# Kernel tuning notes

Measured on AMD Instinct MI355X. Metric: run time of the kernel, lower is better.

The kernel has to match this reference:

```python
import jax, jax.numpy as jnp
import numpy as np

B, L, D, NH, NITEMS = 256, 200, 128, 2, 100000
HD = D // NH
LAMB = 0.6
NEG = -1e9

_PARAM_SHAPES = dict(
    item_emb=(NITEMS, D), pos_emb=(L, D),
    W_ei=(D, D), b_ei=(D,), W_eo=(D, D), b_eo=(D,), b_iah=(D,), b_oah=(D,),
    w_ih=(3 * D, 2 * D), b_ih=(3 * D,), w_hh=(3 * D, D), b_hh=(3 * D,),
    ln1_g=(D,), ln1_b=(D,),
    Wq=(D, D), bq=(D,), Wk=(D, D), bk=(D,), Wv=(D, D), bv=(D,), Wo=(D, D), bo=(D,),
    ln2_g=(D,), ln2_b=(D,), W1=(D, D), b1=(D,), W2=(D, D), b2=(D,),
    lnf_g=(D,), lnf_b=(D,),
)


def setup_inputs() -> dict:
    key = jax.random.key(0)
    ks = jax.random.split(key, len(_PARAM_SHAPES) + 2)
    stdv = 1.0 / np.sqrt(D)  # GCSAN._init_weights: uniform(-stdv, stdv) on ALL params
    p = {}
    for i, (name, shp) in enumerate(_PARAM_SHAPES.items()):
        p[name] = jax.random.uniform(ks[i], shp, jnp.float32, -stdv, stdv)
    lens = jax.random.randint(ks[-2], (B,), L // 4, L + 1)
    vals = jax.random.randint(ks[-1], (B, L), 1, NITEMS)
    # trailing zero padding, as the original break-on-zero loop assumes
    seqs = jnp.where(jnp.arange(L)[None, :] < lens[:, None], vals, 0).astype(jnp.int32)
    p['seqs'] = seqs
    p['lens'] = lens.astype(jnp.int32)
    return p


def _ln(x, g, b):
    mu = x.mean(-1, keepdims=True)
    var = ((x - mu) ** 2).mean(-1, keepdims=True)
    return (x - mu) / jnp.sqrt(var + 1e-5) * g + b


def _build_graph(seqs):
    # Vectorized replacement of _get_slice (per-row np.unique + adjacency build)
    def per_row(seq):
        s = jnp.sort(seq)
        first = jnp.concatenate([jnp.ones((1,), bool), s[1:] != s[:-1]])
        pos = jnp.cumsum(first) - 1  # compaction target of each first-occurrence
        items = jnp.zeros((L,), seq.dtype).at[jnp.where(first, pos, L)].set(s, mode='drop')
        n_u = first.sum()
        search = jnp.where(jnp.arange(L) < n_u, items, jnp.iinfo(jnp.int32).max)
        alias = jnp.searchsorted(search, seq).astype(jnp.int32)
        return items, alias
    items, alias = jax.vmap(per_row)(seqs)
    valid = seqs[:, 1:] > 0  # edge (i -> i+1) exists until first pad
    u = jnp.where(valid, alias[:, :-1], L)  # route masked edges to dummy row L
    v = jnp.where(valid, alias[:, 1:], L)
    bidx = jnp.arange(B)[:, None]
    uA = jnp.zeros((B, L + 1, L + 1), jnp.float32).at[bidx, u, v].set(1.0)[:, :L, :L]
    in_deg = jnp.maximum(uA.sum(1), 1.0)
    out_deg = jnp.maximum(uA.sum(2), 1.0)
    A_in = jnp.swapaxes(uA, 1, 2) / in_deg[:, :, None]   # A[i,j] = uA[j,i]/in_deg[i]
    A_out = uA / out_deg[:, :, None]                     # A[i,k] = uA[i,k]/out_deg[i]
    return alias, jnp.concatenate([A_in, A_out], axis=2), items  # A: [B, L, 2L]


def reference(item_emb, pos_emb, W_ei, b_ei, W_eo, b_eo, b_iah, b_oah,
              w_ih, b_ih, w_hh, b_hh, ln1_g, ln1_b, Wq, bq, Wk, bk, Wv, bv,
              Wo, bo, ln2_g, ln2_b, W1, b1, W2, b2, lnf_g, lnf_b, seqs, lens):
    alias, A, items = _build_graph(seqs)
    hidden = item_emb[items]  # [B, L, D]
    # SR-GNN gated cell, step = n_layers = 1
    for _ in range(1):
        h_in = jnp.einsum('bij,bjd->bid', A[:, :, :L], hidden @ W_ei.T + b_ei) + b_iah
        h_out = jnp.einsum('bij,bjd->bid', A[:, :, L:], hidden @ W_eo.T + b_eo) + b_oah
        gi = jnp.concatenate([h_in, h_out], -1) @ w_ih.T + b_ih
        gh = hidden @ w_hh.T + b_hh
        i_r, i_i, i_n = jnp.split(gi, 3, -1)
        h_r, h_i, h_n = jnp.split(gh, 3, -1)
        r = jax.nn.sigmoid(i_r + h_r)
        z = jax.nn.sigmoid(i_i + h_i)
        ng = jnp.tanh(i_n + r * h_n)
        hidden = ng + z * (hidden - ng)
    bidx = jnp.arange(B)
    seq_hidden = hidden[bidx[:, None], alias]  # alias-gather back to sequence order
    last_idx = lens - 1
    ht = seq_hidden[bidx, last_idx]
    x = seq_hidden + pos_emb[None, :, :]
    tl_mask = (seqs > 0)[:, :, None].astype(x.dtype)
    x = x * tl_mask
    causal = jnp.triu(jnp.ones((L, L), bool), 1)  # True = masked future (bidirectional=False)
    # SASRec-style block: ln -> MHA residual -> ln -> pointwise FFN residual
    q_in = _ln(x, ln1_g, ln1_b)
    heads = lambda t: t.reshape(B, L, NH, HD).transpose(0, 2, 1, 3)
    q = heads(q_in @ Wq.T + bq)
    k = heads(x @ Wk.T + bk)
    v = heads(x @ Wv.T + bv)
    sc = jnp.einsum('bhqd,bhkd->bhqk', q, k) / jnp.sqrt(jnp.asarray(HD, x.dtype))
    sc = jnp.where(causal[None, None], NEG, sc)
    attn = jax.nn.softmax(sc, -1)
    mo = jnp.einsum('bhqk,bhkd->bhqd', attn, v).transpose(0, 2, 1, 3).reshape(B, L, D) @ Wo.T + bo
    x = q_in + mo
    h = _ln(x, ln2_g, ln2_b)
    x = h + jax.nn.relu(h @ W1.T + b1) @ W2.T + b2
    x = x * tl_mask
    log_feats = _ln(x, lnf_g, lnf_b)
    out = log_feats[bidx, last_idx]
    return LAMB * out + (1.0 - LAMB) * ht
```

## Files before the change

### kernel.cpp

```cpp
#include <hip/hip_runtime.h>
#include <hip/hip_bf16.h>

#define Bb 256
#define Ll 200
#define Dd 128
#define BL (Bb*Ll)

typedef __hip_bfloat16 bf16;
typedef __attribute__((ext_vector_type(8))) short short8;
typedef __attribute__((ext_vector_type(4))) unsigned short ushort4v;
typedef __attribute__((ext_vector_type(4))) float floatx4;

__device__ __forceinline__ float b2f(bf16 v) { return __bfloat162float(v); }
__device__ __forceinline__ bf16  f2b(float v) { return __float2bfloat16(v); }
__device__ __forceinline__ float us2f(unsigned short u) { return __uint_as_float(((unsigned)u) << 16); }
__device__ __forceinline__ unsigned short f2us(float v) { bf16 t = f2b(v); return *(unsigned short*)&t; }
__device__ __forceinline__ float ldf(const void* p, int i, int f32) {
  return f32 ? ((const float*)p)[i] : b2f(((const bf16*)p)[i]);
}
__device__ __forceinline__ int detect_f32(const unsigned short* __restrict__ w) {
  unsigned short u = w[threadIdx.x & 63];
  return (__ballot(((u >> 7) & 0xFF) >= 0x7F) != 0ull) ? 1 : 0;
}
__device__ __forceinline__ void load_lds16(const void* g, void* l) {
  __builtin_amdgcn_global_load_lds((const __attribute__((address_space(1))) unsigned int*)g,
                                   (__attribute__((address_space(3))) unsigned int*)l, 16, 0, 0);
}

struct PackP {
  const void *W_ei,*W_eo,*w_ih,*w_hh,*Wk,*Wv,*Wqp,*Wop,*W1p,*W2p,*pos;
  const void *b_ei,*b_eo,*b_ih,*b_hh,*bk,*bv,*bqp,*bop,*b1p,*b2p,*biah,*boah;
  const void *ln1g,*ln1b,*ln2g,*ln2b,*lnfg,*lnfb;
  bf16 *cWhe,*cWih,*cWhh,*cWkv,*cWq,*cWo,*cW1,*cW2,*cPos;
  float *bias_he,*bias_gi,*bias_gh,*bias_kv,*cbq,*cbo,*cb1,*cb2,*cbiah,*cboah,*cln;
  const int* seqs;
  int *alias_g, *items_g; float *rin_g, *rout_g; unsigned *adj_g, *adjT_g;
};
__global__ __launch_bounds__(256) void k01(PackP p) {
  __shared__ alignas(16) int s[Ll];
  __shared__ int al[Ll], its[Ll];
  __shared__ alignas(4) unsigned char isf[Ll];
  __shared__ unsigned adjL[Ll*8], adjTL[Ll*8];
  if (blockIdx.x >= Bb) {
    int idx = (blockIdx.x - Bb) * 256 + threadIdx.x;
    int f32 = detect_f32((const unsigned short*)p.W_ei);
    if (idx < 131072) {
      if (idx < 32768) {
        int r = idx >> 7, c = idx & 127;
        p.cWhe[idx] = f2b(r < 128 ? ldf(p.W_ei, r*128+c, f32) : ldf(p.W_eo, (r-128)*128+c, f32));
      } else p.cWih[idx-32768] = f2b(ldf(p.w_ih, idx-32768, f32));
    } else if (idx < 278528) {
      if (idx < 180224)      p.cWhh[idx-131072] = f2b(ldf(p.w_hh, idx-131072, f32));
      else if (idx < 212992) {
        int i = idx - 180224; int r = i >> 7, c = i & 127;
        p.cWkv[i] = f2b(r < 128 ? ldf(p.Wk, r*128+c, f32) : ldf(p.Wv, (r-128)*128+c, f32));
      }
      else if (idx < 229376) p.cWq[idx-212992] = f2b(ldf(p.Wqp, idx-212992, f32));
      else if (idx < 245760) p.cWo[idx-229376] = f2b(ldf(p.Wop, idx-229376, f32));
      else if (idx < 262144) p.cW1[idx-245760] = f2b(ldf(p.W1p, idx-245760, f32));
      else                   p.cW2[idx-262144] = f2b(ldf(p.W2p, idx-262144, f32));
    } else if (idx < 304128) {
      p.cPos[idx-278528] = f2b(ldf(p.pos, idx-278528, f32));
    } else {
      int j = idx - 304128;
      if      (j < 256)  p.bias_he[j]     = (j<128) ? ldf(p.b_ei,j,f32) : ldf(p.b_eo,j-128,f32);
      else if (j < 640)  p.bias_gi[j-256] = ldf(p.b_ih, j-256, f32);
      else if (j < 1024) p.bias_gh[j-640] = ldf(p.b_hh, j-640, f32);
      else if (j < 1280) { int c=j-1024; p.bias_kv[c] = (c<128)? ldf(p.bk,c,f32): ldf(p.bv,c-128,f32); }
      else if (j < 1408) p.cbq[j-1280]   = ldf(p.bqp, j-1280, f32);
      else if (j < 1536) p.cbo[j-1408]   = ldf(p.bop, j-1408, f32);
      else if (j < 1664) p.cb1[j-1536]   = ldf(p.b1p, j-1536, f32);
      else if (j < 1792) p.cb2[j-1664]   = ldf(p.b2p, j-1664, f32);
      else if (j < 1920) p.cbiah[j-1792] = ldf(p.biah, j-1792, f32);
      else if (j < 2048) p.cboah[j-1920] = ldf(p.boah, j-1920, f32);
      else {
        int i = j - 2048, g = i >> 7, c2 = i & 127;
        const void* s6 = g==0?p.ln1g: g==1?p.ln1b: g==2?p.ln2g: g==3?p.ln2b: g==4?p.lnfg: p.lnfb;
        p.cln[i] = ldf(s6, c2, f32);
      }
    }
    return;
  }
  int b = blockIdx.x, t = threadIdx.x;
  if (t < Ll) s[t] = p.seqs[b*Ll + t];
  for (int i = t; i < Ll*8; i += 256) { adjL[i] = 0u; adjTL[i] = 0u; }
  __syncthreads();
  const int4* s4 = (const int4*)s;
  if (t < Ll) {
    int v = s[t]; int dup = 0;
    int nb = t >> 2;
    for (int j4 = 0; j4 < nb; j4++) {
      int4 sv = s4[j4];
      dup |= (sv.x==v) | (sv.y==v) | (sv.z==v) | (sv.w==v);
    }
    for (int j = nb*4; j < t; j++) dup |= (s[j]==v);
    isf[t] = dup ? 0 : 1; its[t] = 0;
  }
  __syncthreads();
  const unsigned* isfw = (const unsigned*)isf;
  if (t < Ll) {
    int v = s[t], r = 0;
    for (int j4 = 0; j4 < Ll/4; j4++) {
      int4 sv = s4[j4];
      unsigned fw = isfw[j4];
      r += ((fw & 0xffu)       && sv.x < v);
      r += ((fw & 0xff00u)     && sv.y < v);
      r += ((fw & 0xff0000u)   && sv.z < v);
      r += ((fw & 0xff000000u) && sv.w < v);
    }
    al[t] = r;
  }
  __syncthreads();
  if (t < Ll && isf[t]) its[al[t]] = s[t];
  if (t < Ll-1 && s[t+1] > 0) {
    int u = al[t], v = al[t+1];
    atomicOr(&adjL [u*8 + (v >> 5)], 1u << (v & 31));
    atomicOr(&adjTL[v*8 + (u >> 5)], 1u << (u & 31));
  }
  __syncthreads();
  if (t < Ll) {
    int od = 0, id = 0;
    for (int wd = 0; wd < 7; wd++) { od += __popc(adjL[t*8+wd]); id += __popc(adjTL[t*8+wd]); }
    p.rout_g [b*Ll + t] = 1.0f / (float)max(od, 1);
    p.rin_g  [b*Ll + t] = 1.0f / (float)max(id, 1);
    p.alias_g[b*Ll + t] = al[t];
    p.items_g[b*Ll + t] = its[t];
  }
  for (int i = t; i < Ll*8; i += 256) { p.adj_g[b*Ll*8 + i] = adjL[i]; p.adjT_g[b*Ll*8 + i] = adjTL[i]; }
}

__global__ __launch_bounds__(256) void k2_gather(const void* __restrict__ emb, const void* __restrict__ wei,
    const int* __restrict__ items_g, bf16* __restrict__ hidden)
{
  int idx = blockIdx.x * 256 + threadIdx.x;
  int f32 = detect_f32((const unsigned short*)wei);
  int n = idx >> 4, jv = idx & 15;
  int it = items_g[n];
  short8 o;
  if (f32) {
    const float* e = (const float*)emb + (size_t)it * 128 + jv * 8;
#pragma unroll
    for (int j = 0; j < 8; j++) o[j] = (short)f2us(e[j]);
  } else {
    o = ((const short8*)((const bf16*)emb + (size_t)it * 128))[jv];
  }
  ((short8*)hidden)[idx] = o;
}

template<int K>
__global__ __launch_bounds__(256) void gemm6(const bf16* __restrict__ A, const bf16* __restrict__ W,
    const float* __restrict__ bias,
    bf16* __restrict__ out_lo, int Nlo, bf16* __restrict__ out_hi, int Nhi, int split)
{
  __shared__ short As[128*128];
  __shared__ short Ws[128*128];
  int t = threadIdx.x;
  int wave = t >> 6, lane = t & 63;
  int q = lane >> 4, mr = lane & 15;
  int wm = wave & 1, wn = wave >> 1;
  int m0 = blockIdx.x * 128, n0 = blockIdx.y * 128;
  int srow = lane >> 4;
  int c16 = lane & 15;
  floatx4 acc[4][4] = {};
  for (int k0 = 0; k0 < K; k0 += 128) {
#pragma unroll
    for (int i = 0; i < 8; i++) {
      int seg = wave*8 + i;
      int r = seg*4 + srow;
      int gch = c16 ^ (r & 15);
      load_lds16(A + (size_t)(m0 + r) * K + k0 + gch*8, &As[seg*512]);
      load_lds16(W + (size_t)(n0 + r) * K + k0 + gch*8, &Ws[seg*512]);
    }
    __syncthreads();
#pragma unroll
    for (int kk = 0; kk < 4; kk++) {
      short8 af[4], wf[4];
#pragma unroll
      for (int i = 0; i < 4; i++) {
        int row = wm*64 + i*16 + mr;
        af[i] = *(const short8*)(&As[row*128 + ((kk*4+q) ^ (row&15))*8]);
      }
#pragma unroll
      for (int j = 0; j < 4; j++) {
        int row = wn*64 + j*16 + mr;
        wf[j] = *(const short8*)(&Ws[row*128 + ((kk*4+q) ^ (row&15))*8]);
      }
#pragma unroll
      for (int i = 0; i < 4; i++)
#pragma unroll
        for (int j = 0; j < 4; j++)
          acc[i][j] = __builtin_amdgcn_mfma_f32_16x16x32_bf16(wf[j], af[i], acc[i][j], 0, 0, 0);
    }
    if (k0 + 128 < K) __syncthreads();
  }
#pragma unroll
  for (int j = 0; j < 4; j++) {
    int ng = n0 + wn*64 + j*16 + q*4;
    floatx4 bs = *(const floatx4*)(bias + ng);
    bf16* outp; int col, stride;
    if (ng < split) { outp = out_lo; col = ng; stride = Nlo; }
    else            { outp = out_hi; col = ng - split; stride = Nhi; }
#pragma unroll
    for (int i = 0; i < 4; i++) {
      int m = m0 + wm*64 + i*16 + mr;
      ushort4v o;
#pragma unroll
      for (int e = 0; e < 4; e++) o[e] = f2us(acc[i][j][e] + bs[e]);
      *(ushort4v*)(outp + (size_t)m * stride + col) = o;
    }
  }
}

__global__ __launch_bounds__(256) void k3_agg(const bf16* __restrict__ he,
    const unsigned* __restrict__ adj_g, const unsigned* __restrict__ adjT_g,
    const float* __restrict__ rin_g, const float* __restrict__ rout_g,
    const float* __restrict__ cbiah, const float* __restrict__ cboah, bf16* __restrict__ hio)
{
  int b = blockIdx.x / 25, chunk = blockIdx.x % 25;
  int wave = threadIdx.x >> 6, lane = threadIdx.x & 63;
  bool isIn = lane < 32;
  int c = isIn ? 4*lane : 128 + 4*(lane-32);
  const bf16* heb = he + (size_t)b * Ll * 256;
  bf16* hiob = hio + (size_t)b * Ll * 256;
  float bias0 = isIn ? cbiah[c]   : cboah[c-128];
  float bias1 = isIn ? cbiah[c+1] : cboah[c-127];
  float bias2 = isIn ? cbiah[c+2] : cboah[c-126];
  float bias3 = isIn ? cbiah[c+3] : cboah[c-125];
#pragma unroll
  for (int s = 0; s < 2; s++) {
    int i = chunk*8 + wave + 4*s;
    const unsigned* mrow = (isIn ? adjT_g : adj_g) + ((size_t)b*Ll + i) * 8;
    float a0=0.f, a1=0.f, a2=0.f, a3=0.f;
    for (int wd = 0; wd < 7; wd++) {
      unsigned bits = mrow[wd];
      while (bits) {
        int j = (wd << 5) + __builtin_ctz(bits); bits &= bits - 1;
        ushort4v h4 = *(const ushort4v*)(heb + (size_t)j*256 + c);
        a0 += us2f(h4.x); a1 += us2f(h4.y); a2 += us2f(h4.z); a3 += us2f(h4.w);
      }
    }
    float r = isIn ? rin_g[b*Ll + i] : rout_g[b*Ll + i];
    ushort4v o;
    o.x = f2us(bias0 + r*a0); o.y = f2us(bias1 + r*a1);
    o.z = f2us(bias2 + r*a2); o.w = f2us(bias3 + r*a3);
    *(ushort4v*)(hiob + (size_t)i*256 + c) = o;
  }
}

__global__ __launch_bounds__(256) void k45(const bf16* __restrict__ gi, const bf16* __restrict__ gh,
    const bf16* __restrict__ hidden, const int* __restrict__ alias_g,
    const int* __restrict__ seqs, const int* __restrict__ lens,
    const bf16* __restrict__ cPos, bf16* __restrict__ x, float* __restrict__ ht)
{
  __shared__ bf16 hnew[Ll*64];
  __shared__ int aliasL[Ll];
  __shared__ unsigned char validL[Ll];
  int b = blockIdx.x >> 1, half = blockIdx.x & 1;
  int t = threadIdx.x;
  if (t < Ll) { aliasL[t] = alias_g[b*Ll + t]; validL[t] = seqs[b*Ll + t] > 0; }
  int li = lens[b] - 1;
  for (int u = t; u < Ll*8; u += 256) {
    int n = u >> 3, grp = u & 7;
    int j8 = half*8 + grp;
    const short8* gin = (const short8*)(gi + ((size_t)b*Ll + n) * 384);
    const short8* ghn = (const short8*)(gh + ((size_t)b*Ll + n) * 384);
    short8 vir = gin[j8], vii = gin[16+j8], vnn = gin[32+j8];
    short8 whr = ghn[j8], whi = ghn[16+j8], whn = ghn[32+j8];
    short8 hv  = ((const short8*)(hidden + ((size_t)b*Ll + n) * Dd))[j8];
    short8 o;
#pragma unroll
    for (int e = 0; e < 8; e++) {
      float ir = us2f((unsigned short)vir[e]), ii = us2f((unsigned short)vii[e]), inn = us2f((unsigned short)vnn[e]);
      float hr = us2f((unsigned short)whr[e]), hi = us2f((unsigned short)whi[e]), hn = us2f((unsigned short)whn[e]);
      float r  = 1.f / (1.f + __expf(-(ir + hr)));
      float z  = 1.f / (1.f + __expf(-(ii + hi)));
      float arg = inn + r * hn;
      float ex = __expf(-2.f * arg);
      float ng = (1.f - ex) / (1.f + ex);
      float h  = us2f((unsigned short)hv[e]);
      o[e] = (short)f2us(ng + z * (h - ng));
    }
    *(short8*)&hnew[n*64 + grp*8] = o;
  }
  __syncthreads();
  for (int u = t; u < Ll*8; u += 256) {
    int tpos = u >> 3, grp = u & 7;
    int a = aliasL[tpos];
    short8 sh8 = *(const short8*)&hnew[a*64 + grp*8];
    short8 pv = ((const short8*)(cPos + tpos * Dd))[half*8 + grp];
    bool valid = validL[tpos];
    bool isLast = (tpos == li);
    short8 o;
#pragma unroll
    for (int e = 0; e < 8; e++) {
      float sh = us2f((unsigned short)sh8[e]);
      o[e] = valid ? (short)f2us(sh + us2f((unsigned short)pv[e])) : (short)0;
      if (isLast) ht[b*Dd + half*64 + grp*8 + e] = sh;
    }
    ((short8*)(x + ((size_t)b*Ll + tpos) * Dd))[half*8 + grp] = o;
  }
}

struct FinalP {
  const bf16 *x, *kv; const float* ht;
  const bf16 *cWq, *cWo, *cW1, *cW2;
  const float *cbq, *cbo, *cb1, *cb2, *cln;
  const int* lens; const void* wei;
  void* out;
};
__device__ __forceinline__ float dot128i(const bf16* __restrict__ wrow, const float* __restrict__ vin) {
  const short8* wr = (const short8*)wrow;
  float a0=0.f, a1=0.f, a2=0.f, a3=0.f;
#pragma unroll
  for (int kk = 0; kk < 4; kk++) {
    short8 w0 = wr[kk*4+0], w1 = wr[kk*4+1], w2 = wr[kk*4+2], w3 = wr[kk*4+3];
#pragma unroll
    for (int j = 0; j < 8; j++) {
      a0 += vin[kk*32 +      j] * us2f((unsigned short)w0[j]);
      a1 += vin[kk*32 + 8  + j] * us2f((unsigned short)w1[j]);
      a2 += vin[kk*32 + 16 + j] * us2f((unsigned short)w2[j]);
      a3 += vin[kk*32 + 24 + j] * us2f((unsigned short)w3[j]);
    }
  }
  return (a0+a1)+(a2+a3);
}
__device__ __forceinline__ float wave_sum(float v) {
#pragma unroll
  for (int m = 1; m < 64; m <<= 1) v += __shfl_xor(v, m, 64);
  return v;
}
__device__ __forceinline__ float wave_max(float v) {
#pragma unroll
  for (int m = 1; m < 64; m <<= 1) v = fmaxf(v, __shfl_xor(v, m, 64));
  return v;
}
__global__ __launch_bounds__(256) void k7_final(FinalP p)
{
  __shared__ float sred[8];
  __shared__ float qin[128], qv[128], aout[128], hh[128], f1[128];
  __shared__ float pb0[256], pb1[256];
  __shared__ floatx4 av4[8][32];
  int b = blockIdx.x, t = threadIdx.x, c = t;
  int w = t >> 6, ln = t & 63;
  int li = p.lens[b] - 1;
  int f32 = detect_f32((const unsigned short*)p.wei);
  float xv = (c < 128) ? b2f(p.x[((size_t)b*Ll + li) * Dd + c]) : 0.f;
  float s = wave_sum(xv), s2 = wave_sum(xv*xv);
  if (ln == 0) { sred[w] = s; sred[4+w] = s2; }
  __syncthreads();
  float mu = (sred[0]+sred[1]+sred[2]+sred[3]) * (1.f/128.f);
  float ms = (sred[4]+sred[5]+sred[6]+sred[7]) * (1.f/128.f);
  float rs = rsqrtf(fmaxf(ms - mu*mu, 0.f) + 1e-5f);
  __syncthreads();
  if (c < 128) qin[c] = (xv - mu) * rs * p.cln[c] + p.cln[128+c];
  __syncthreads();
  if (c < 128) qv[c] = p.cbq[c] + dot128i(p.cWq + c*128, qin);
  __syncthreads();
  const bf16* kvb = p.kv + (size_t)b * Ll * 256;
  float s0 = -3.0e38f, s1 = -3.0e38f;
  if (t <= li) {
    const short8* kr = (const short8*)(kvb + (size_t)t*256);
    float a00=0.f,a01=0.f,a10=0.f,a11=0.f;
#pragma unroll
    for (int kk = 0; kk < 4; kk++) {
      short8 k0 = kr[kk*2], k1 = kr[kk*2+1], k2 = kr[8+kk*2], k3 = kr[8+kk*2+1];
#pragma unroll
      for (int j = 0; j < 8; j++) {
        a00 += qv[kk*16 + j]      * us2f((unsigned short)k0[j]);
        a01 += qv[kk*16 + 8 + j]  * us2f((unsigned short)k1[j]);
        a10 += qv[64 + kk*16 + j]     * us2f((unsigned short)k2[j]);
        a11 += qv[64 + kk*16 + 8 + j] * us2f((unsigned short)k3[j]);
      }
    }
    s0 = (a00+a01) * 0.125f; s1 = (a10+a11) * 0.125f;
  }
  float m0 = wave_max(s0), m1 = wave_max(s1);
  if (ln == 0) { sred[w] = m0; sred[4+w] = m1; }
  __syncthreads();
  m0 = fmaxf(fmaxf(sred[0],sred[1]), fmaxf(sred[2],sred[3]));
  m1 = fmaxf(fmaxf(sred[4],sred[5]), fmaxf(sred[6],sred[7]));
  __syncthreads();
  float e0 = (t <= li) ? __expf(s0 - m0) : 0.f;
  float e1 = (t <= li) ? __expf(s1 - m1) : 0.f;
  pb0[t] = e0; pb1[t] = e1;
  float l0 = wave_sum(e0), l1 = wave_sum(e1);
  if (ln == 0) { sred[w] = l0; sred[4+w] = l1; }
  __syncthreads();
  l0 = sred[0]+sred[1]+sred[2]+sred[3];
  l1 = sred[4]+sred[5]+sred[6]+sred[7];
  {
    int part = t >> 5, cq = t & 31, ch = cq * 4;
    int cnt = li + 1, cpp = (cnt + 7) >> 3;
    int j0 = part * cpp, j1 = min(j0 + cpp, cnt);
    const float* pbh = (ch < 64) ? pb0 : pb1;
    float a0=0.f,a1=0.f,a2=0.f,a3=0.f;
#pragma unroll 4
    for (int j = j0; j < j1; j++) {
      ushort4v v4 = *(const ushort4v*)(kvb + (size_t)j*256 + 128 + ch);
      float pw = pbh[j];
      a0 += pw*us2f(v4.x); a1 += pw*us2f(v4.y); a2 += pw*us2f(v4.z); a3 += pw*us2f(v4.w);
    }
    floatx4 o = {a0,a1,a2,a3};
    av4[part][cq] = o;
  }
  __syncthreads();
  if (c < 128) {
    float l = (c < 64) ? l0 : l1;
    float acc = 0.f;
#pragma unroll
    for (int pp = 0; pp < 8; pp++) acc += ((const float*)&av4[pp][c>>2])[c&3];
    aout[c] = acc / l;
  }
  __syncthreads();
  float x2v = 0.f;
  if (c < 128) x2v = qin[c] + p.cbo[c] + dot128i(p.cWo + c*128, aout);
  s = wave_sum((c<128)?x2v:0.f); s2 = wave_sum((c<128)?x2v*x2v:0.f);
  if (ln == 0) { sred[w] = s; sred[4+w] = s2; }
  __syncthreads();
  mu = (sred[0]+sred[1]+sred[2]+sred[3]) * (1.f/128.f);
  ms = (sred[4]+sred[5]+sred[6]+sred[7]) * (1.f/128.f);
  rs = rsqrtf(fmaxf(ms - mu*mu, 0.f) + 1e-5f);
  __syncthreads();
  if (c < 128) hh[c] = (x2v - mu) * rs * p.cln[256+c] + p.cln[384+c];
  __syncthreads();
  if (c < 128) f1[c] = fmaxf(p.cb1[c] + dot128i(p.cW1 + c*128, hh), 0.f);
  __syncthreads();
  float x3v = 0.f;
  if (c < 128) x3v = hh[c] + p.cb2[c] + dot128i(p.cW2 + c*128, f1);
  s = wave_sum((c<128)?x3v:0.f); s2 = wave_sum((c<128)?x3v*x3v:0.f);
  if (ln == 0) { sred[w] = s; sred[4+w] = s2; }
  __syncthreads();
  mu = (sred[0]+sred[1]+sred[2]+sred[3]) * (1.f/128.f);
  ms = (sred[4]+sred[5]+sred[6]+sred[7]) * (1.f/128.f);
  rs = rsqrtf(fmaxf(ms - mu*mu, 0.f) + 1e-5f);
  if (c < 128) {
    float lf = (x3v - mu) * rs * p.cln[512+c] + p.cln[640+c];
    float outv = 0.6f * lf + 0.4f * p.ht[b*Dd + c];
    if (f32) ((float*)p.out)[b*Dd + c] = outv;
    else     ((bf16*)p.out)[b*Dd + c]  = f2b(outv);
  }
}

extern "C" void kernel_launch(void* const* d_in, const int* in_sizes, int n_in,
                              void* d_out, int out_size, void* d_ws, size_t ws_size,
                              hipStream_t stream)
{
  (void)in_sizes; (void)n_in; (void)out_size; (void)ws_size;
  const void* item_emb = d_in[0];
  const int* seqs = (const int*)d_in[30];
  const int* lens = (const int*)d_in[31];

  char* wsp = (char*)d_ws;
  size_t o = 0;
  auto alloc = [&](size_t sz) { void* p = wsp + o; o += (sz + 255) & ~(size_t)255; return p; };
  int*      alias_g = (int*)alloc((size_t)BL*4);
  int*      items_g = (int*)alloc((size_t)BL*4);
  float*    rin_g   = (float*)alloc((size_t)BL*4);
  float*    rout_g  = (float*)alloc((size_t)BL*4);
  unsigned* adj_g   = (unsigned*)alloc((size_t)BL*8*4);
  unsigned* adjT_g  = (unsigned*)alloc((size_t)BL*8*4);
  float*    ht_g    = (float*)alloc((size_t)Bb*Dd*4);
  bf16*     cWhe    = (bf16*)alloc(32768*2);
  bf16*     cWhh    = (bf16*)alloc(49152*2);
  bf16*     cWih    = (bf16*)alloc(98304*2);
  bf16*     cWkv    = (bf16*)alloc(32768*2);
  bf16*     cWq     = (bf16*)alloc(16384*2);
  bf16*     cWo     = (bf16*)alloc(16384*2);
  bf16*     cW1     = (bf16*)alloc(16384*2);
  bf16*     cW2     = (bf16*)alloc(16384*2);
  bf16*     cPos    = (bf16*)alloc(25600*2);
  float*    bias_he = (float*)alloc(256*4);
  float*    bias_gh = (float*)alloc(384*4);
  float*    bias_gi = (float*)alloc(384*4);
  float*    bias_kv = (float*)alloc(256*4);
  float*    cbq     = (float*)alloc(128*4);
  float*    cbo     = (float*)alloc(128*4);
  float*    cb1     = (float*)alloc(128*4);
  float*    cb2     = (float*)alloc(128*4);
  float*    cbiah   = (float*)alloc(128*4);
  float*    cboah   = (float*)alloc(128*4);
  float*    cln     = (float*)alloc(768*4);
  bf16*     hidden  = (bf16*)alloc((size_t)BL*128*2);
  bf16*     he      = (bf16*)alloc((size_t)BL*256*2);
  bf16*     hio     = (bf16*)alloc((size_t)BL*256*2);
  bf16*     gi      = (bf16*)alloc((size_t)BL*384*2);
  bf16*     gh      = (bf16*)alloc((size_t)BL*384*2);
  bf16*     x  = he;
  bf16*     kv = hio;

  PackP pp = { d_in[2], d_in[4], d_in[8], d_in[10], d_in[16], d_in[18], d_in[14], d_in[20],
               d_in[24], d_in[26], d_in[1],
               d_in[3], d_in[5], d_in[9], d_in[11], d_in[17], d_in[19], d_in[15], d_in[21],
               d_in[25], d_in[27], d_in[6], d_in[7],
               d_in[12], d_in[13], d_in[22], d_in[23], d_in[28], d_in[29],
               cWhe, cWih, cWhh, cWkv, cWq, cWo, cW1, cW2, cPos,
               bias_he, bias_gi, bias_gh, bias_kv, cbq, cbo, cb1, cb2, cbiah, cboah, cln,
               seqs, alias_g, items_g, rin_g, rout_g, adj_g, adjT_g };
  k01<<<Bb + 1199, 256, 0, stream>>>(pp);
  k2_gather<<<BL*16/256, 256, 0, stream>>>(item_emb, d_in[2], items_g, hidden);
  gemm6<128><<<dim3(BL/128, 5), 256, 0, stream>>>(hidden, cWhe, bias_he, he, 256, gh, 384, 256);
  k3_agg<<<Bb*25, 256, 0, stream>>>(he, adj_g, adjT_g, rin_g, rout_g, cbiah, cboah, hio);
  gemm6<256><<<dim3(BL/128, 3), 256, 0, stream>>>(hio, cWih, bias_gi, gi, 384, gi, 384, 1<<30);
  k45<<<Bb*2, 256, 0, stream>>>(gi, gh, hidden, alias_g, seqs, lens, cPos, x, ht_g);
  gemm6<128><<<dim3(BL/128, 2), 256, 0, stream>>>(x, cWkv, bias_kv, kv, 256, kv, 256, 1<<30);
  FinalP fp = { x, kv, ht_g, cWq, cWo, cW1, cW2, cbq, cbo, cb1, cb2, cln, lens, d_in[2], d_out };
  k7_final<<<Bb, 256, 0, stream>>>(fp);
}
```

Measured before the change: 280.1 us.

## Fuse GRU gate, alias gather and KV projection into one per-batch kernel

The GRU gate kernel and the separate KV GEMM are replaced by one kernel per batch row. It computes the gated hidden state directly at alias positions, adds the positional embedding into an LDS tile, and runs the 256x128 KV projection with MFMA from LDS, keeping the weight fragments in registers. The final kernel rebuilds the last-position input from ht plus cPos, so x is never written to global memory. This removes one launch and the global round trip of x. In exchange the padding mask is no longer applied to K/V rows, which relies on the last-query attention only reading positions up to len-1, and the grid is only 256 blocks.

```diff
diff --git a/kernel.cpp b/kernel.cpp
--- a/kernel.cpp
+++ b/kernel.cpp
@@ -247,26 +247,29 @@
   }
 }
 
-__global__ __launch_bounds__(256) void k45(const bf16* __restrict__ gi, const bf16* __restrict__ gh,
-    const bf16* __restrict__ hidden, const int* __restrict__ alias_g,
-    const int* __restrict__ seqs, const int* __restrict__ lens,
-    const bf16* __restrict__ cPos, bf16* __restrict__ x, float* __restrict__ ht)
+__global__ __launch_bounds__(256) void kv_fused(const bf16* __restrict__ gi, const bf16* __restrict__ gh,
+    const bf16* __restrict__ hidden, const int* __restrict__ alias_g, const int* __restrict__ lens,
+    const bf16* __restrict__ cPos, const bf16* __restrict__ cWkv, const float* __restrict__ bias_kv,
+    bf16* __restrict__ kv, float* __restrict__ ht)
 {
-  __shared__ bf16 hnew[Ll*64];
+  __shared__ short xs[208*136];
   __shared__ int aliasL[Ll];
-  __shared__ unsigned char validL[Ll];
-  int b = blockIdx.x >> 1, half = blockIdx.x & 1;
-  int t = threadIdx.x;
-  if (t < Ll) { aliasL[t] = alias_g[b*Ll + t]; validL[t] = seqs[b*Ll + t] > 0; }
+  int b = blockIdx.x, t = threadIdx.x;
+  int wave = t >> 6, lane = t & 63, q = lane >> 4, mr = lane & 15;
   int li = lens[b] - 1;
-  for (int u = t; u < Ll*8; u += 256) {
-    int n = u >> 3, grp = u & 7;
-    int j8 = half*8 + grp;
-    const short8* gin = (const short8*)(gi + ((size_t)b*Ll + n) * 384);
-    const short8* ghn = (const short8*)(gh + ((size_t)b*Ll + n) * 384);
-    short8 vir = gin[j8], vii = gin[16+j8], vnn = gin[32+j8];
-    short8 whr = ghn[j8], whi = ghn[16+j8], whn = ghn[32+j8];
-    short8 hv  = ((const short8*)(hidden + ((size_t)b*Ll + n) * Dd))[j8];
+  if (t < Ll) aliasL[t] = alias_g[b*Ll + t];
+  for (int u = t; u < 8*136; u += 256) xs[Ll*136 + u] = 0;
+  __syncthreads();
+  for (int u = t; u < Ll*16; u += 256) {
+    int tpos = u >> 4, jv = u & 15;
+    int a = aliasL[tpos];
+    const short8* gin = (const short8*)(gi + ((size_t)b*Ll + a) * 384);
+    const short8* ghn = (const short8*)(gh + ((size_t)b*Ll + a) * 384);
+    short8 vir = gin[jv], vii = gin[16+jv], vnn = gin[32+jv];
+    short8 whr = ghn[jv], whi = ghn[16+jv], whn = ghn[32+jv];
+    short8 hv  = ((const short8*)(hidden + ((size_t)b*Ll + a) * Dd))[jv];
+    short8 pv  = ((const short8*)(cPos + tpos * Dd))[jv];
+    bool isLast = (tpos == li);
     short8 o;
 #pragma unroll
     for (int e = 0; e < 8; e++) {
@@ -278,31 +281,49 @@
       float ex = __expf(-2.f * arg);
       float ng = (1.f - ex) / (1.f + ex);
       float h  = us2f((unsigned short)hv[e]);
-      o[e] = (short)f2us(ng + z * (h - ng));
-    }
-    *(short8*)&hnew[n*64 + grp*8] = o;
-  }
-  __syncthreads();
-  for (int u = t; u < Ll*8; u += 256) {
-    int tpos = u >> 3, grp = u & 7;
-    int a = aliasL[tpos];
-    short8 sh8 = *(const short8*)&hnew[a*64 + grp*8];
-    short8 pv = ((const short8*)(cPos + tpos * Dd))[half*8 + grp];
-    bool valid = validL[tpos];
-    bool isLast = (tpos == li);
-    short8 o;
-#pragma unroll
-    for (int e = 0; e < 8; e++) {
-      float sh = us2f((unsigned short)sh8[e]);
-      o[e] = valid ? (short)f2us(sh + us2f((unsigned short)pv[e])) : (short)0;
-      if (isLast) ht[b*Dd + half*64 + grp*8 + e] = sh;
-    }
-    ((short8*)(x + ((size_t)b*Ll + tpos) * Dd))[half*8 + grp] = o;
+      float sh = ng + z * (h - ng);
+      o[e] = (short)f2us(sh + us2f((unsigned short)pv[e]));
+      if (isLast) ht[b*Dd + jv*8 + e] = sh;
+    }
+    *(short8*)&xs[tpos*136 + jv*8] = o;
+  }
+  __syncthreads();
+  short8 wf[4][4];
+#pragma unroll
+  for (int kk = 0; kk < 4; kk++)
+#pragma unroll
+    for (int j = 0; j < 4; j++) {
+      int n = wave*64 + j*16 + mr;
+      wf[kk][j] = *(const short8*)(cWkv + (size_t)n*128 + kk*32 + q*8);
+    }
+  for (int mt = 0; mt < 13; mt++) {
+    short8 af[4];
+#pragma unroll
+    for (int kk = 0; kk < 4; kk++)
+      af[kk] = *(const short8*)&xs[(mt*16 + mr)*136 + (kk*4+q)*8];
+    floatx4 acc[4] = {};
+#pragma unroll
+    for (int kk = 0; kk < 4; kk++)
+#pragma unroll
+      for (int j = 0; j < 4; j++)
+        acc[j] = __builtin_amdgcn_mfma_f32_16x16x32_bf16(wf[kk][j], af[kk], acc[j], 0, 0, 0);
+    int m = mt*16 + mr;
+    if (m < Ll) {
+#pragma unroll
+      for (int j = 0; j < 4; j++) {
+        int n = wave*64 + j*16 + q*4;
+        floatx4 bs = *(const floatx4*)(bias_kv + n);
+        ushort4v o;
+#pragma unroll
+        for (int e = 0; e < 4; e++) o[e] = f2us(acc[j][e] + bs[e]);
+        *(ushort4v*)(kv + ((size_t)b*Ll + m)*256 + n) = o;
+      }
+    }
   }
 }
 
 struct FinalP {
-  const bf16 *x, *kv; const float* ht;
+  const bf16 *kv; const float* ht; const bf16* cPos;
   const bf16 *cWq, *cWo, *cW1, *cW2;
   const float *cbq, *cbo, *cb1, *cb2, *cln;
   const int* lens; const void* wei;
@@ -344,7 +365,7 @@
   int w = t >> 6, ln = t & 63;
   int li = p.lens[b] - 1;
   int f32 = detect_f32((const unsigned short*)p.wei);
-  float xv = (c < 128) ? b2f(p.x[((size_t)b*Ll + li) * Dd + c]) : 0.f;
+  float xv = (c < 128) ? (p.ht[b*Dd + c] + b2f(p.cPos[li*Dd + c])) : 0.f;
   float s = wave_sum(xv), s2 = wave_sum(xv*xv);
   if (ln == 0) { sred[w] = s; sred[4+w] = s2; }
   __syncthreads();
@@ -485,7 +506,6 @@
   bf16*     hio     = (bf16*)alloc((size_t)BL*256*2);
   bf16*     gi      = (bf16*)alloc((size_t)BL*384*2);
   bf16*     gh      = (bf16*)alloc((size_t)BL*384*2);
-  bf16*     x  = he;
   bf16*     kv = hio;
 
   PackP pp = { d_in[2], d_in[4], d_in[8], d_in[10], d_in[16], d_in[18], d_in[14], d_in[20],
@@ -501,8 +521,7 @@
   gemm6<128><<<dim3(BL/128, 5), 256, 0, stream>>>(hidden, cWhe, bias_he, he, 256, gh, 384, 256);
   k3_agg<<<Bb*25, 256, 0, stream>>>(he, adj_g, adjT_g, rin_g, rout_g, cbiah, cboah, hio);
   gemm6<256><<<dim3(BL/128, 3), 256, 0, stream>>>(hio, cWih, bias_gi, gi, 384, gi, 384, 1<<30);
-  k45<<<Bb*2, 256, 0, stream>>>(gi, gh, hidden, alias_g, seqs, lens, cPos, x, ht_g);
-  gemm6<128><<<dim3(BL/128, 2), 256, 0, stream>>>(x, cWkv, bias_kv, kv, 256, kv, 256, 1<<30);
-  FinalP fp = { x, kv, ht_g, cWq, cWo, cW1, cW2, cbq, cbo, cb1, cb2, cln, lens, d_in[2], d_out };
+  kv_fused<<<Bb, 256, 0, stream>>>(gi, gh, hidden, alias_g, lens, cPos, cWkv, bias_kv, kv, ht_g);
+  FinalP fp = { kv, ht_g, cPos, cWq, cWo, cW1, cW2, cbq, cbo, cb1, cb2, cln, lens, d_in[2], d_out };
   k7_final<<<Bb, 256, 0, stream>>>(fp);
 }
```

Measured after the change: 276.1 us. No clear change (-1.4%).
